# Kernel optimization log

Measured on AMD Instinct MI355X. Metric: run time of the kernel, lower is better.

Reference implementation:

```python
import jax, jax.numpy as jnp
import numpy as np

ALPHA = 100.0  # self.softmax_alpha


def _interp_nearest(x, size):
    # torch F.interpolate mode='nearest': src_idx = floor(dst_idx * H_in / H_out)
    H, W = x.shape[-2], x.shape[-1]
    h, w = size
    ri = (jnp.arange(h) * H) // h
    ci = (jnp.arange(w) * W) // w
    return x[:, :, ri, :][:, :, :, ci]


def _interp_bilinear_ac(x, size):
    # torch F.interpolate mode='bilinear', align_corners=True
    H, W = x.shape[-2], x.shape[-1]
    h, w = size

    def coords(n_out, n_in):
        if n_out == 1:
            return jnp.zeros((1,), jnp.float32)
        return jnp.arange(n_out, dtype=jnp.float32) * ((n_in - 1) / (n_out - 1))

    ry, rx = coords(h, H), coords(w, W)
    y0 = jnp.floor(ry).astype(jnp.int32)
    x0 = jnp.floor(rx).astype(jnp.int32)
    y1 = jnp.clip(y0 + 1, 0, H - 1)
    x1 = jnp.clip(x0 + 1, 0, W - 1)
    wy = (ry - y0.astype(jnp.float32))[None, None, :, None]
    wx = (rx - x0.astype(jnp.float32))[None, None, None, :]
    rows = x[:, :, y0, :] * (1.0 - wy) + x[:, :, y1, :] * wy  # (n,c,h,W)
    return rows[:, :, :, x0] * (1.0 - wx) + rows[:, :, :, x1] * wx  # (n,c,h,w)


def _warp(unalign_fb, fa, fa_parse, fb, fb_parse, alpha):
    n, c, h, w = fa.shape
    c2 = unalign_fb.shape[1]
    hw = h * w
    # center and channel-normalize features per spatial location
    fa = fa - jnp.mean(fa, axis=(2, 3), keepdims=True)
    fb = fb - jnp.mean(fb, axis=(2, 3), keepdims=True)
    fa = fa.reshape(n, c, hw)
    fb = fb.reshape(n, c, hw)
    fa = fa / jnp.linalg.norm(fa, axis=1, keepdims=True)
    fb = fb / jnp.linalg.norm(fb, axis=1, keepdims=True)
    ufb = unalign_fb.reshape(n, c2, hw)
    mask_a = (fa_parse.reshape(n, -1, hw)[:, 1:, :] != 0).astype(fa.dtype)  # (n,K,hw)
    mask_b = (fb_parse.reshape(n, -1, hw)[:, 1:, :] != 0).astype(fb.dtype)
    local_fa = fa[:, None, :, :] * mask_a[:, :, None, :]  # (n,K,c,hw)
    local_fb = fb[:, None, :, :] * mask_b[:, :, None, :]  # (n,K,c,hw)
    # energy[n,k,q,p] = sum_c local_fb[n,k,c,q] * local_fa[n,k,c,p]
    energy = jnp.einsum('nkcq,nkcp->nkqp', local_fb, local_fa) * alpha
    corr = jax.nn.softmax(energy, axis=2)  # softmax over fb locations q
    warped = jnp.einsum('ncq,nkqp->nkcp', ufb, corr)  # (n,K,c2,hw)
    combined = (warped * mask_a[:, :, None, :]).sum(axis=1)  # (n,c2,hw)
    norm = jnp.maximum(mask_a.sum(axis=1, keepdims=True), 1.0)  # (n,1,hw)
    aligned = combined / norm
    return aligned.reshape(n, c2, h, w)


def setup_inputs() -> dict:
    key = jax.random.key(0)
    k1, k2, k3, k4, k5 = jax.random.split(key, 5)
    return {
        'unalign_fb': jax.random.normal(k1, (1, 64, 256, 256), jnp.float32),
        'fa': jax.random.normal(k2, (1, 256, 64, 64), jnp.float32),
        'fa_parse': jax.random.randint(k3, (1, 4, 256, 256), 0, 2).astype(jnp.int32),
        'fb': jax.random.normal(k4, (1, 256, 64, 64), jnp.float32),
        'fb_parse': jax.random.randint(k5, (1, 4, 256, 256), 0, 2).astype(jnp.int32),
    }


def reference(unalign_fb, fa, fa_parse, fb, fb_parse):
    raw_hw = unalign_fb.shape[-2:]
    feat_hw = fa.shape[-2:]
    fa_p = _interp_nearest(fa_parse, feat_hw)
    fb_p = _interp_nearest(fb_parse, feat_hw)
    ufb = _interp_bilinear_ac(unalign_fb, fb.shape[-2:])
    aligned = _warp(ufb, fa, fa_p, fb, fb_p, ALPHA)
    return _interp_bilinear_ac(aligned, raw_hw)
```

## Files before the change

kernel.cpp:

```cpp
#include <hip/hip_runtime.h>
#include <math.h>

#define HW 4096
#define CC 256
#define C2 64
#define E50f 1.928749848e-22f

typedef unsigned short USH;
typedef __attribute__((ext_vector_type(8))) _Float16 f16x8;
typedef __attribute__((ext_vector_type(8))) short bf8;
typedef __attribute__((ext_vector_type(4))) float f32x4;

__device__ __forceinline__ USH f2bf(float x) {
    unsigned u = __float_as_uint(x);
    u += 0x7fff + ((u >> 16) & 1);
    return (USH)(u >> 16);
}
__device__ __forceinline__ USH f2h(float x) {
    _Float16 h = (_Float16)x;
    return *(USH*)&h;
}

__device__ __forceinline__ void gl2lds16(const USH* g, USH* l) {
    __builtin_amdgcn_global_load_lds(
        (const __attribute__((address_space(1))) void*)g,
        (__attribute__((address_space(3))) void*)l, 16, 0, 0);
}

__global__ void k_prep1(const float* __restrict__ fa, const float* __restrict__ fb,
                        float* __restrict__ mu,
                        const float* __restrict__ ufb_src, const int* __restrict__ fb_parse,
                        USH* __restrict__ vtT, float* __restrict__ bgp) {
    __shared__ float4 sred[256];
    int t = threadIdx.x;
    if (blockIdx.x < 512) {
        int b = blockIdx.x;
        const float* src = (b < CC) ? (fa + b * HW) : (fb + (b - CC) * HW);
        float s = 0.f;
        for (int q = t; q < HW; q += 256) s += src[q];
        sred[t].x = s;
        __syncthreads();
        for (int st = 128; st > 0; st >>= 1) {
            if (t < st) sred[t].x += sred[t + st].x;
            __syncthreads();
        }
        if (t == 0) mu[b] = sred[0].x * (1.0f / HW);
        return;
    }
    int bid = blockIdx.x - 512;
    int pblk = bid & 15, c = bid >> 4;
    int p = pblk * 256 + t;
    int j = p >> 6, i = p & 63;
    int off = (4 * j) * 256 + 4 * i;
    float m0 = (fb_parse[1 * 65536 + off] != 0) ? 1.f : 0.f;
    float m1 = (fb_parse[2 * 65536 + off] != 0) ? 1.f : 0.f;
    float m2 = (fb_parse[3 * 65536 + off] != 0) ? 1.f : 0.f;
    float ry = j * (255.0f / 63.0f);
    int y0 = (int)ry; y0 = min(y0, 255); int y1 = min(y0 + 1, 255);
    float wy = ry - (float)y0;
    float rx = i * (255.0f / 63.0f);
    int x0 = (int)rx; x0 = min(x0, 255); int x1 = min(x0 + 1, 255);
    float wx = rx - (float)x0;
    const float* sc = ufb_src + c * 65536;
    float r0 = sc[y0 * 256 + x0] * (1.f - wx) + sc[y0 * 256 + x1] * wx;
    float r1 = sc[y1 * 256 + x0] * (1.f - wx) + sc[y1 * 256 + x1] * wx;
    float v = r0 * (1.f - wy) + r1 * wy;
    size_t cbase = (size_t)(p >> 5) * 8192 + (p & 31);
    vtT[cbase + (0 * 65 + c) * 32] = f2bf(v * m0);
    vtT[cbase + (1 * 65 + c) * 32] = f2bf(v * m1);
    vtT[cbase + (2 * 65 + c) * 32] = f2bf(v * m2);
    if (c == 0) {
        vtT[cbase + 64 * 32]  = f2bf(m0);
        vtT[cbase + 129 * 32] = f2bf(m1);
        vtT[cbase + 194 * 32] = f2bf(m2);
        for (int m = 195; m < 256; ++m) vtT[cbase + m * 32] = 0;
    }
    sred[t] = make_float4(v, v * m0, v * m1, v * m2);
    __syncthreads();
    for (int st = 128; st > 0; st >>= 1) {
        if (t < st) {
            float4 o = sred[t + st];
            sred[t].x += o.x; sred[t].y += o.y; sred[t].z += o.z; sred[t].w += o.w;
        }
        __syncthreads();
    }
    if (t == 0) {
        float4 r = sred[0];
        bgp[pblk * 320 + 256 + c]     = r.x;
        bgp[pblk * 320 + 0 * 65 + c]  = r.y;
        bgp[pblk * 320 + 1 * 65 + c]  = r.z;
        bgp[pblk * 320 + 2 * 65 + c]  = r.w;
    }
    __syncthreads();
    if (c == 0) {
        sred[t] = make_float4(m0, m1, m2, 0.f);
        __syncthreads();
        for (int st = 128; st > 0; st >>= 1) {
            if (t < st) {
                float4 o = sred[t + st];
                sred[t].x += o.x; sred[t].y += o.y; sred[t].z += o.z;
            }
            __syncthreads();
        }
        if (t == 0) {
            float4 r = sred[0];
            bgp[pblk * 320 + 64]  = r.x;
            bgp[pblk * 320 + 129] = r.y;
            bgp[pblk * 320 + 194] = r.z;
        }
    }
}

__global__ void k_norm_ss(const float* __restrict__ fa, const float* __restrict__ fb,
                          const float* __restrict__ mu, float* __restrict__ ssq_part) {
    int which = blockIdx.z;
    const float* src = which ? fb : fa;
    int p = blockIdx.x * 256 + threadIdx.x;
    int c0 = blockIdx.y * 32;
    float ss = 0.f;
    for (int c = c0; c < c0 + 32; ++c) {
        float v = src[c * HW + p] - mu[which * CC + c];
        ss += v * v;
    }
    ssq_part[(which * 8 + blockIdx.y) * HW + p] = ss;
}

__global__ __launch_bounds__(256) void k_norm_split_t(
    const float* __restrict__ fa, const float* __restrict__ fb,
    const float* __restrict__ mu, const float* __restrict__ ssq_part,
    USH* __restrict__ faT, USH* __restrict__ fbT) {
    __shared__ float tile[64][68];
    int which = blockIdx.z;
    const float* src = which ? fb : fa;
    USH* dst = which ? fbT : faT;
    int p0 = blockIdx.x * 64;
    int c0 = blockIdx.y * 64;
    int t = threadIdx.x;
    {
        int c_r = t >> 2, seg = t & 3;
        const float* s = &src[(size_t)(c0 + c_r) * HW + p0 + seg * 16];
#pragma unroll
        for (int k = 0; k < 4; ++k)
            *(float4*)&tile[c_r][seg * 16 + k * 4] = *(const float4*)&s[k * 4];
    }
    __syncthreads();
    {
        int p_r = t >> 2, seg = t & 3;
        int cl = seg * 16;
        float ss = 0.f;
#pragma unroll
        for (int z = 0; z < 8; ++z) ss += ssq_part[(which * 8 + z) * HW + p0 + p_r];
        float rinv = rsqrtf(ss);
        union { USH us[8]; uint4 v; } h0, h1;
#pragma unroll
        for (int j = 0; j < 8; ++j)
            h0.us[j] = f2h((tile[cl + j][p_r] - mu[which * CC + c0 + cl + j]) * rinv);
#pragma unroll
        for (int j = 0; j < 8; ++j)
            h1.us[j] = f2h((tile[cl + 8 + j][p_r] - mu[which * CC + c0 + cl + 8 + j]) * rinv);
        int kc = (c0 >> 5) + (seg >> 1);
        size_t base = (size_t)kc * 131072 + (size_t)(p0 + p_r) * 32 + (seg & 1) * 16;
        *(uint4*)&dst[base] = h0.v;
        *(uint4*)&dst[base + 8] = h1.v;
    }
}

__global__ __launch_bounds__(256, 2) void k_attn(
    const USH* __restrict__ faT, const USH* __restrict__ fbT,
    const USH* __restrict__ vtT, float* __restrict__ part) {
    __shared__ USH sA[8 * 2048];
    __shared__ USH sE[64 * 136];
    int t = threadIdx.x;
    int bid = blockIdx.x;
    int z = bid & 7;
    int p0 = (bid >> 3) * 64;
    int w = t >> 6, lane = t & 63, lr = lane & 15, quad = lane >> 4;
    f32x4 accp[4][4] = {};

#pragma unroll
    for (int kk = 0; kk < 2; ++kk) {
        int kc = 2 * w + kk;
#pragma unroll
        for (int seg = 0; seg < 4; ++seg)
            gl2lds16(faT + (size_t)kc * 131072 + (size_t)p0 * 32 + seg * 512 + lane * 8,
                     &sA[kc * 2048 + seg * 512]);
    }

    const USH* pB = fbT + (size_t)(z * 512 + 32 * w + lr) * 32 + quad * 8;
    const USH* pV = vtT + (size_t)(64 * w + lr) * 32 + quad * 8;

    __syncthreads();

    for (int qt = 0; qt < 4; ++qt) {
        f32x4 accs[2][4] = {};
#pragma unroll
        for (int kc = 0; kc < 8; ++kc) {
            f16x8 a[2], b[4];
#pragma unroll
            for (int i = 0; i < 2; ++i)
                a[i] = *(const f16x8*)&pB[(size_t)kc * 131072 + qt * 4096 + i * 512];
#pragma unroll
            for (int jj = 0; jj < 4; ++jj)
                b[jj] = *(const f16x8*)&sA[kc * 2048 + (16 * jj + lr) * 32 + quad * 8];
#pragma unroll
            for (int i = 0; i < 2; ++i)
#pragma unroll
                for (int jj = 0; jj < 4; ++jj)
                    accs[i][jj] = __builtin_amdgcn_mfma_f32_16x16x32_f16(a[i], b[jj], accs[i][jj], 0, 0, 0);
        }
        if (qt) __syncthreads();
#pragma unroll
        for (int i = 0; i < 2; ++i)
#pragma unroll
            for (int jj = 0; jj < 4; ++jj) {
                unsigned u0 = ((unsigned)f2bf(__expf(fmaf(100.f, accs[i][jj][1], -50.f))) << 16)
                            | (unsigned)f2bf(__expf(fmaf(100.f, accs[i][jj][0], -50.f)));
                unsigned u1 = ((unsigned)f2bf(__expf(fmaf(100.f, accs[i][jj][3], -50.f))) << 16)
                            | (unsigned)f2bf(__expf(fmaf(100.f, accs[i][jj][2], -50.f)));
                int addr = (16 * jj + lr) * 136 + 32 * w + 16 * i + 4 * quad;
                uint2 u; u.x = u0; u.y = u1;
                *(uint2*)&sE[addr] = u;
            }
        __syncthreads();
#pragma unroll
        for (int kc = 0; kc < 4; ++kc) {
            size_t vb = (size_t)(z * 16 + qt * 4 + kc) * 8192;
            bf8 av[4] = {}, be[4];
#pragma unroll
            for (int i = 0; i < 4; ++i)
                if (!(w == 3 && i > 0))
                    av[i] = *(const bf8*)&pV[vb + i * 512];
#pragma unroll
            for (int jj = 0; jj < 4; ++jj)
                be[jj] = *(const bf8*)&sE[(16 * jj + lr) * 136 + kc * 32 + quad * 8];
#pragma unroll
            for (int i = 0; i < 4; ++i)
#pragma unroll
                for (int jj = 0; jj < 4; ++jj)
                    if (!(w == 3 && i > 0))
                        accp[i][jj] = __builtin_amdgcn_mfma_f32_16x16x32_bf16(av[i], be[jj], accp[i][jj], 0, 0, 0);
        }
    }
    float* op = part + (size_t)z * 1048576;
#pragma unroll
    for (int i = 0; i < 4; ++i) {
        int m = 64 * w + 16 * i + quad * 4;
#pragma unroll
        for (int jj = 0; jj < 4; ++jj) {
            int pc = p0 + 16 * jj + lr;
#pragma unroll
            for (int r = 0; r < 4; ++r)
                if (m + r < 195)
                    op[(size_t)(m + r) * HW + pc] = accp[i][jj][r];
        }
    }
}

__global__ void k_combine8(const float* __restrict__ part, const float* __restrict__ bgp,
                           const int* __restrict__ fa_parse, float* __restrict__ aligned) {
    __shared__ float sums[8];
    int t = threadIdx.x;
    int c2 = blockIdx.y;
    if (t < 7) {
        int idx = (t < 3) ? (t * 65 + 64) : ((t < 6) ? (t - 3) * 65 + c2 : 256 + c2);
        float s = 0.f;
#pragma unroll
        for (int pb = 0; pb < 16; ++pb) s += bgp[pb * 320 + idx];
        sums[t] = s;
    }
    __syncthreads();
    int p = blockIdx.x * 256 + t;
    int jj = p >> 6, ii = p & 63;
    int off = (4 * jj) * 256 + 4 * ii;
    float num = 0.f, s = 0.f;
    for (int k = 0; k < 3; ++k) {
        float ma = (fa_parse[(k + 1) * 65536 + off] != 0) ? 1.f : 0.f;
        s += ma;
        float den = E50f * (4096.0f - sums[k]);
        float nu  = E50f * (sums[6] - sums[3 + k]);
        size_t rd = (size_t)(k * 65 + 64) * HW + p;
        size_t rn = (size_t)(k * 65 + c2) * HW + p;
#pragma unroll
        for (int z = 0; z < 8; ++z) {
            den += part[(size_t)z * 1048576 + rd];
            nu  += part[(size_t)z * 1048576 + rn];
        }
        num += ma * (nu / den);
    }
    aligned[c2 * HW + p] = num / fmaxf(s, 1.f);
}

__global__ void k_bilin_up(const float* __restrict__ aligned, float* __restrict__ out) {
    int idx = (blockIdx.x * 256 + threadIdx.x) * 4;
    int c2 = blockIdx.y;
    int y = idx >> 8;
    float ry = y * (63.0f / 255.0f);
    int y0 = (int)ry; y0 = min(y0, 63); int y1 = min(y0 + 1, 63);
    float wy = ry - (float)y0;
    const float* a = aligned + c2 * HW;
    float4 o;
    float* op = &o.x;
#pragma unroll
    for (int u = 0; u < 4; ++u) {
        int x = (idx & 255) + u;
        float rx = x * (63.0f / 255.0f);
        int x0 = (int)rx; x0 = min(x0, 63); int x1 = min(x0 + 1, 63);
        float wx = rx - (float)x0;
        float r0 = a[y0 * 64 + x0] * (1.f - wx) + a[y0 * 64 + x1] * wx;
        float r1 = a[y1 * 64 + x0] * (1.f - wx) + a[y1 * 64 + x1] * wx;
        op[u] = r0 * (1.f - wy) + r1 * wy;
    }
    *(float4*)&out[c2 * 65536 + idx] = o;
}

extern "C" void kernel_launch(void* const* d_in, const int* in_sizes, int n_in,
                              void* d_out, int out_size, void* d_ws, size_t ws_size,
                              hipStream_t stream) {
    const float* unalign_fb = (const float*)d_in[0];
    const float* fa         = (const float*)d_in[1];
    const int*   fa_parse   = (const int*)d_in[2];
    const float* fb         = (const float*)d_in[3];
    const int*   fb_parse   = (const int*)d_in[4];
    float* out = (float*)d_out;

    float* w = (float*)d_ws;
    float* mu       = w;
    float* ssq_part = w + 512;
    float* bgp      = w + 66048;
    float* part     = w + 71168;
    float* aligned  = w + 8459776;
    USH* faT = (USH*)(w + 8721920);
    USH* fbT = (USH*)(w + 9246208);
    USH* vtT = (USH*)(w + 9770496);

    k_prep1<<<dim3(1536), dim3(256), 0, stream>>>(fa, fb, mu, unalign_fb, fb_parse, vtT, bgp);
    k_norm_ss<<<dim3(16, 8, 2), dim3(256), 0, stream>>>(fa, fb, mu, ssq_part);
    k_norm_split_t<<<dim3(64, 4, 2), dim3(256), 0, stream>>>(fa, fb, mu, ssq_part, faT, fbT);
    k_attn<<<dim3(512), dim3(256), 0, stream>>>(faT, fbT, vtT, part);
    k_combine8<<<dim3(16, 64), dim3(256), 0, stream>>>(part, bgp, fa_parse, aligned);
    k_bilin_up<<<dim3(64, 64), dim3(256), 0, stream>>>(aligned, out);
}
```

Baseline: 130.2 us.

## Fuse norm sum-of-squares into transpose kernel and batch combine over channels

Merges the separate sum-of-squares pass and the normalize/transpose kernel into one kernel where each block holds all 256 channels for 32 positions in shared memory, reduces the norm in-block, then writes fp16 transposed output. This removes a launch and a second global read of fa/fb plus the ssq_part round trip. Separately, k_combine8 now processes 4 output channels per block, so the denominator partial sums and parse masks are loaded once per 4 channels instead of per channel. The fused kernel launches only 256 blocks with scalar loads, which may lower memory parallelism.

Result: no change. 130.2 us (+0.0%).

```diff
diff --git a/kernel.cpp b/kernel.cpp
--- a/kernel.cpp
+++ b/kernel.cpp
@@ -111,57 +111,49 @@
     }
 }
 
-__global__ void k_norm_ss(const float* __restrict__ fa, const float* __restrict__ fb,
-                          const float* __restrict__ mu, float* __restrict__ ssq_part) {
-    int which = blockIdx.z;
-    const float* src = which ? fb : fa;
-    int p = blockIdx.x * 256 + threadIdx.x;
-    int c0 = blockIdx.y * 32;
-    float ss = 0.f;
-    for (int c = c0; c < c0 + 32; ++c) {
-        float v = src[c * HW + p] - mu[which * CC + c];
-        ss += v * v;
-    }
-    ssq_part[(which * 8 + blockIdx.y) * HW + p] = ss;
-}
-
-__global__ __launch_bounds__(256) void k_norm_split_t(
+__global__ __launch_bounds__(256) void k_normT(
     const float* __restrict__ fa, const float* __restrict__ fb,
-    const float* __restrict__ mu, const float* __restrict__ ssq_part,
+    const float* __restrict__ mu_,
     USH* __restrict__ faT, USH* __restrict__ fbT) {
-    __shared__ float tile[64][68];
+    __shared__ float tile[256][33];
+    __shared__ float red[8][32];
+    __shared__ float rv[32];
     int which = blockIdx.z;
     const float* src = which ? fb : fa;
     USH* dst = which ? fbT : faT;
-    int p0 = blockIdx.x * 64;
-    int c0 = blockIdx.y * 64;
+    const float* mu = mu_ + which * CC;
+    int p0 = blockIdx.x * 32;
     int t = threadIdx.x;
-    {
-        int c_r = t >> 2, seg = t & 3;
-        const float* s = &src[(size_t)(c0 + c_r) * HW + p0 + seg * 16];
-#pragma unroll
-        for (int k = 0; k < 4; ++k)
-            *(float4*)&tile[c_r][seg * 16 + k * 4] = *(const float4*)&s[k * 4];
-    }
-    __syncthreads();
-    {
-        int p_r = t >> 2, seg = t & 3;
-        int cl = seg * 16;
-        float ss = 0.f;
-#pragma unroll
-        for (int z = 0; z < 8; ++z) ss += ssq_part[(which * 8 + z) * HW + p0 + p_r];
-        float rinv = rsqrtf(ss);
-        union { USH us[8]; uint4 v; } h0, h1;
-#pragma unroll
-        for (int j = 0; j < 8; ++j)
-            h0.us[j] = f2h((tile[cl + j][p_r] - mu[which * CC + c0 + cl + j]) * rinv);
-#pragma unroll
-        for (int j = 0; j < 8; ++j)
-            h1.us[j] = f2h((tile[cl + 8 + j][p_r] - mu[which * CC + c0 + cl + 8 + j]) * rinv);
-        int kc = (c0 >> 5) + (seg >> 1);
-        size_t base = (size_t)kc * 131072 + (size_t)(p0 + p_r) * 32 + (seg & 1) * 16;
-        *(uint4*)&dst[base] = h0.v;
-        *(uint4*)&dst[base + 8] = h1.v;
+    int pi = t & 31, g = t >> 5;
+    for (int it = 0; it < 32; ++it) {
+        int c = it * 8 + g;
+        tile[c][pi] = src[(size_t)c * HW + p0 + pi];
+    }
+    __syncthreads();
+    float ss = 0.f;
+#pragma unroll
+    for (int jc = 0; jc < 32; ++jc) {
+        float v = tile[g * 32 + jc][pi] - mu[g * 32 + jc];
+        ss += v * v;
+    }
+    red[g][pi] = ss;
+    __syncthreads();
+    if (g == 0) {
+        float s2 = 0.f;
+#pragma unroll
+        for (int gg = 0; gg < 8; ++gg) s2 += red[gg][pi];
+        rv[pi] = rsqrtf(s2);
+    }
+    __syncthreads();
+    float rinv = rv[pi];
+    size_t base = (size_t)g * 131072 + (size_t)(p0 + pi) * 32;
+#pragma unroll
+    for (int seg = 0; seg < 4; ++seg) {
+        union { USH us[8]; uint4 v; } h;
+#pragma unroll
+        for (int jc = 0; jc < 8; ++jc)
+            h.us[jc] = f2h((tile[g * 32 + seg * 8 + jc][pi] - mu[g * 32 + seg * 8 + jc]) * rinv);
+        *(uint4*)&dst[base + seg * 8] = h.v;
     }
 }
 
@@ -258,36 +250,53 @@
 
 __global__ void k_combine8(const float* __restrict__ part, const float* __restrict__ bgp,
                            const int* __restrict__ fa_parse, float* __restrict__ aligned) {
-    __shared__ float sums[8];
+    __shared__ float sden[3];
+    __shared__ float sc2[4][4];
     int t = threadIdx.x;
-    int c2 = blockIdx.y;
-    if (t < 7) {
-        int idx = (t < 3) ? (t * 65 + 64) : ((t < 6) ? (t - 3) * 65 + c2 : 256 + c2);
+    int cg = blockIdx.y * 4;
+    if (t < 19) {
+        int idx;
+        if (t < 3) idx = t * 65 + 64;
+        else {
+            int lc = (t - 3) >> 2, r = (t - 3) & 3;
+            idx = (r < 3) ? r * 65 + (cg + lc) : 256 + (cg + lc);
+        }
         float s = 0.f;
 #pragma unroll
         for (int pb = 0; pb < 16; ++pb) s += bgp[pb * 320 + idx];
-        sums[t] = s;
+        if (t < 3) sden[t] = s;
+        else sc2[(t - 3) >> 2][(t - 3) & 3] = s;
     }
     __syncthreads();
     int p = blockIdx.x * 256 + t;
     int jj = p >> 6, ii = p & 63;
     int off = (4 * jj) * 256 + 4 * ii;
-    float num = 0.f, s = 0.f;
+    float ma[3], den[3];
+    float s = 0.f;
+#pragma unroll
     for (int k = 0; k < 3; ++k) {
-        float ma = (fa_parse[(k + 1) * 65536 + off] != 0) ? 1.f : 0.f;
-        s += ma;
-        float den = E50f * (4096.0f - sums[k]);
-        float nu  = E50f * (sums[6] - sums[3 + k]);
+        ma[k] = (fa_parse[(k + 1) * 65536 + off] != 0) ? 1.f : 0.f;
+        s += ma[k];
+        den[k] = E50f * (4096.0f - sden[k]);
         size_t rd = (size_t)(k * 65 + 64) * HW + p;
-        size_t rn = (size_t)(k * 65 + c2) * HW + p;
-#pragma unroll
-        for (int z = 0; z < 8; ++z) {
-            den += part[(size_t)z * 1048576 + rd];
-            nu  += part[(size_t)z * 1048576 + rn];
-        }
-        num += ma * (nu / den);
-    }
-    aligned[c2 * HW + p] = num / fmaxf(s, 1.f);
+#pragma unroll
+        for (int z = 0; z < 8; ++z) den[k] += part[(size_t)z * 1048576 + rd];
+    }
+    float fs = fmaxf(s, 1.f);
+#pragma unroll
+    for (int lc = 0; lc < 4; ++lc) {
+        int c2 = cg + lc;
+        float num = 0.f;
+#pragma unroll
+        for (int k = 0; k < 3; ++k) {
+            float nu = E50f * (sc2[lc][3] - sc2[lc][k]);
+            size_t rn = (size_t)(k * 65 + c2) * HW + p;
+#pragma unroll
+            for (int z = 0; z < 8; ++z) nu += part[(size_t)z * 1048576 + rn];
+            num += ma[k] * (nu / den[k]);
+        }
+        aligned[(size_t)c2 * HW + p] = num / fs;
+    }
 }
 
 __global__ void k_bilin_up(const float* __restrict__ aligned, float* __restrict__ out) {
@@ -325,7 +334,6 @@
 
     float* w = (float*)d_ws;
     float* mu       = w;
-    float* ssq_part = w + 512;
     float* bgp      = w + 66048;
     float* part     = w + 71168;
     float* aligned  = w + 8459776;
@@ -334,9 +342,8 @@
     USH* vtT = (USH*)(w + 9770496);
 
     k_prep1<<<dim3(1536), dim3(256), 0, stream>>>(fa, fb, mu, unalign_fb, fb_parse, vtT, bgp);
-    k_norm_ss<<<dim3(16, 8, 2), dim3(256), 0, stream>>>(fa, fb, mu, ssq_part);
-    k_norm_split_t<<<dim3(64, 4, 2), dim3(256), 0, stream>>>(fa, fb, mu, ssq_part, faT, fbT);
+    k_normT<<<dim3(128, 1, 2), dim3(256), 0, stream>>>(fa, fb, mu, faT, fbT);
     k_attn<<<dim3(512), dim3(256), 0, stream>>>(faT, fbT, vtT, part);
-    k_combine8<<<dim3(16, 64), dim3(256), 0, stream>>>(part, bgp, fa_parse, aligned);
+    k_combine8<<<dim3(16, 16), dim3(256), 0, stream>>>(part, bgp, fa_parse, aligned);
     k_bilin_up<<<dim3(64, 64), dim3(256), 0, stream>>>(aligned, out);
 }
```
